# Kernel optimization log

Measured on AMD Instinct MI355X. Metric: run time of the kernel, lower is better.

The kernel has to match this reference:

```python
import jax, jax.numpy as jnp
import numpy as np

WINDOW = 11  # sliding window width (odd)


def setup_inputs() -> dict:
    key = jax.random.key(0)
    k1, k2, k3 = jax.random.split(key, 3)
    LENGTH, RANK = 200000, 64
    time_factor = jax.random.normal(k1, (LENGTH, RANK), dtype=jnp.float32)
    # nn.Linear(RANK, RANK): weight (out,in), bias (out,)
    W = jax.random.normal(k2, (RANK, RANK), dtype=jnp.float32) / np.sqrt(RANK)
    b = jax.random.normal(k3, (RANK,), dtype=jnp.float32) * 0.01
    return {"time_factor": time_factor, "W": W, "b": b}


def reference(time_factor, W, b):
    row, col = time_factor.shape
    pad = (WINDOW - 1) // 2
    # F.pad on transposed data pads the row (time) dimension with zeros
    padded = jnp.pad(time_factor, ((pad, pad), (0, 0)))
    # indexer: blocks[i] = padded[i : i+WINDOW]  -> (row, WINDOW, col)
    idx = jnp.arange(row)[:, None] + jnp.arange(WINDOW)[None, :]
    blocks = padded[idx]
    # var1 = tanh(Linear(data))  (exp contains '_tanh')
    var1 = jnp.tanh(time_factor @ W.T + b)            # (row, col)
    # var2 = bmm(blocks, var1) -> per-row window scores
    var2 = jnp.einsum('rwc,rc->rw', blocks, var1)      # (row, WINDOW)
    # exp ends with 'scaled'
    var2 = var2 / jnp.sqrt(jnp.asarray(col, time_factor.dtype))
    # exp starts with 'softmax' (softmax over window dim)
    var2 = jax.nn.softmax(var2, axis=1)
    # var3 = bmm(scores, blocks) -> smoothed factor
    out = jnp.einsum('rw,rwc->rc', var2, blocks)       # (row, col)
    return out
```

## Files before the change

kernel.cpp:

```cpp
#include <hip/hip_runtime.h>
#include <hip/hip_bf16.h>


constexpr int RANK   = 64;
constexpr int WINDOW = 11;
constexpr int PAD    = 5;
constexpr int TILE   = 16;
constexpr int BLOCK  = 256;
constexpr int TR     = 64;
constexpr int BROWS  = 28;
constexpr int BSTR   = 68;
constexpr int SC_S   = 18;
constexpr int GRIDB  = 1024;

constexpr int BAND_F = BROWS * BSTR;
constexpr int SC_OFF = 4 * BAND_F;
constexpr int SMEMF  = SC_OFF + 4 * 32 * SC_S;

typedef short short8  __attribute__((ext_vector_type(8)));
typedef float float4v __attribute__((ext_vector_type(4)));

__device__ __forceinline__ short8 cvt_bf8(float4 a, float4 b) {
    union { short8 s; __hip_bfloat162 h[4]; } u;
    u.h[0] = __float22bfloat162_rn(make_float2(a.x, a.y));
    u.h[1] = __float22bfloat162_rn(make_float2(a.z, a.w));
    u.h[2] = __float22bfloat162_rn(make_float2(b.x, b.y));
    u.h[3] = __float22bfloat162_rn(make_float2(b.z, b.w));
    return u.s;
}

__device__ __forceinline__ float fast_tanh(float x) {
    return 1.0f - 2.0f / (1.0f + __expf(2.0f * x));
}

__global__ __launch_bounds__(BLOCK)
__attribute__((amdgpu_waves_per_eu(4, 4)))
void attn_win_kernel(
    const float* __restrict__ A,
    const float* __restrict__ W,
    const float* __restrict__ b,
    float* __restrict__ out,
    int rows)
{
    __shared__ __align__(16) float smem[SMEMF];

    const int lane = threadIdx.x & 63;
    const int wv   = threadIdx.x >> 6;
    const int m16  = lane & 15;
    const int quad = lane >> 4;
    const int sr   = lane >> 4;
    const int sc4  = (lane & 15) * 4;

    float* const bandW = smem + wv * BAND_F;
    float* const ScW   = smem + SC_OFF + wv * 32 * SC_S;

    short8 wfrag[4][2];
    #pragma unroll
    for (int ct = 0; ct < 4; ct++) {
        #pragma unroll
        for (int kf = 0; kf < 2; kf++) {
            const float4* p =
                (const float4*)(W + (ct * 16 + m16) * RANK + kf * 32 + quad * 8);
            wfrag[ct][kf] = cvt_bf8(p[0], p[1]);
        }
    }
    float4 biasT[4];
    #pragma unroll
    for (int ct = 0; ct < 4; ct++)
        biasT[ct] = *(const float4*)(b + ct * 16 + quad * 4);

    const int idxA = 4 * m16 + 128 * (quad & 1);
    const int idxB = idxA + 64;

    const int n_btiles = (rows + TR - 1) / TR;
    int bt = blockIdx.x;
    if (bt >= n_btiles) return;

    {
        const int rw0 = bt * TR + wv * TILE;
        #pragma unroll
        for (int ro = 0; ro < 7; ro++) {
            const int g = rw0 - PAD + ro * 4 + sr;
            float4 x = make_float4(0.f, 0.f, 0.f, 0.f);
            if ((unsigned)g < (unsigned)rows)
                x = *(const float4*)(A + (size_t)g * RANK + sc4);
            *(float4*)&bandW[(ro * 4 + sr) * BSTR + sc4] = x;
        }
    }

    for (; bt < n_btiles; bt += gridDim.x) {
        const int rw = bt * TR + wv * TILE;

        short8 am1[2];
        #pragma unroll
        for (int kf = 0; kf < 2; kf++) {
            const float4* pp =
                (const float4*)&bandW[(PAD + m16) * BSTR + kf * 32 + quad * 8];
            am1[kf] = cvt_bf8(pp[0], pp[1]);
        }

        float4v accT[4];
        #pragma unroll
        for (int ct = 0; ct < 4; ct++)
            accT[ct] = (float4v){biasT[ct].x, biasT[ct].y,
                                 biasT[ct].z, biasT[ct].w};
        #pragma unroll
        for (int kf = 0; kf < 2; kf++)
            #pragma unroll
            for (int ct = 0; ct < 4; ct++)
                accT[ct] = __builtin_amdgcn_mfma_f32_16x16x32_bf16(
                    wfrag[ct][kf], am1[kf], accT[ct], 0, 0, 0);

        int pk[4][2];
        #pragma unroll
        for (int ct = 0; ct < 4; ct++)
            #pragma unroll
            for (int u = 0; u < 2; u++) {
                union { __hip_bfloat162 h; int i; } cv;
                cv.h = __float22bfloat162_rn(make_float2(
                    fast_tanh(accT[ct][2 * u]),
                    fast_tanh(accT[ct][2 * u + 1])));
                pk[ct][u] = cv.i;
            }

        short8 bfr[2];
        #pragma unroll
        for (int kf = 0; kf < 2; kf++) {
            union { int w[4]; short8 s; } u;
            #pragma unroll
            for (int w = 0; w < 4; w++) {
                const int idx = (w >> 1) ? idxB : idxA;
                const int lo = __builtin_amdgcn_ds_bpermute(idx, pk[2 * kf][w & 1]);
                const int hi = __builtin_amdgcn_ds_bpermute(idx, pk[2 * kf + 1][w & 1]);
                u.w[w] = (quad >= 2) ? hi : lo;
            }
            bfr[kf] = u.s;
        }

        short8 abnd[2][2];
        #pragma unroll
        for (int it = 0; it < 2; it++)
            #pragma unroll
            for (int kf = 0; kf < 2; kf++) {
                const float4* pp = (const float4*)
                    &bandW[(it * 16 + m16) * BSTR + kf * 32 + quad * 8];
                abnd[it][kf] = cvt_bf8(pp[0], pp[1]);
            }

        float4v sacc[2];
        sacc[0] = (float4v){0.f, 0.f, 0.f, 0.f};
        sacc[1] = (float4v){0.f, 0.f, 0.f, 0.f};
        #pragma unroll
        for (int kf = 0; kf < 2; kf++)
            #pragma unroll
            for (int it = 0; it < 2; it++)
                sacc[it] = __builtin_amdgcn_mfma_f32_16x16x32_bf16(
                    abnd[it][kf], bfr[kf], sacc[it], 0, 0, 0);

        #pragma unroll
        for (int it = 0; it < 2; it++)
            #pragma unroll
            for (int rg = 0; rg < 4; rg++)
                ScW[(it * 16 + quad * 4 + rg) * SC_S + m16] = sacc[it][rg];

        float4 stg[7];
        {
            const int rwn = rw + (int)gridDim.x * TR;
            #pragma unroll
            for (int ro = 0; ro < 7; ro++) {
                const int g = rwn - PAD + ro * 4 + sr;
                stg[ro] = make_float4(0.f, 0.f, 0.f, 0.f);
                if ((unsigned)g < (unsigned)rows)
                    stg[ro] = *(const float4*)(A + (size_t)g * RANK + sc4);
            }
        }

        float p[WINDOW];
        {
            float s[WINDOW];
            float mx = -1e30f;
            #pragma unroll
            for (int w = 0; w < WINDOW; w++) {
                s[w] = ScW[(m16 + w) * SC_S + m16];
                mx = fmaxf(mx, s[w]);
            }
            float den = 0.0f;
            #pragma unroll
            for (int w = 0; w < WINDOW; w++) {
                p[w] = __expf((s[w] - mx) * 0.125f);
                den += p[w];
            }
            const float rden = __fdividef(1.0f, den);
            #pragma unroll
            for (int w = 0; w < WINDOW; w++) p[w] *= rden;
        }

        float aw[26];
        #pragma unroll
        for (int s = 0; s < 26; s++) aw[s] = bandW[s * BSTR + lane];

        #pragma unroll
        for (int ro = 0; ro < 7; ro++)
            *(float4*)&bandW[(ro * 4 + sr) * BSTR + sc4] = stg[ro];

        #pragma unroll
        for (int rr = 0; rr < TILE; rr++) {
            float o = 0.0f;
            #pragma unroll
            for (int w = 0; w < WINDOW; w++) {
                const float pw = __uint_as_float(
                    __builtin_amdgcn_readlane(__float_as_uint(p[w]), rr));
                o = fmaf(pw, aw[rr + w], o);
            }
            if (rw + rr < rows)
                out[(size_t)(rw + rr) * RANK + lane] = o;
        }
    }
}

extern "C" void kernel_launch(void* const* d_in, const int* in_sizes, int n_in,
                              void* d_out, int out_size, void* d_ws, size_t ws_size,
                              hipStream_t stream) {
    const float* A = (const float*)d_in[0];
    const float* W = (const float*)d_in[1];
    const float* b = (const float*)d_in[2];
    float* out = (float*)d_out;

    const int rows     = in_sizes[0] / RANK;
    const int n_btiles = (rows + TR - 1) / TR;
    const int blocks   = n_btiles < GRIDB ? n_btiles : GRIDB;

    hipLaunchKernelGGL(attn_win_kernel, dim3(blocks), dim3(BLOCK), 0, stream,
                       A, W, b, out, rows);
}
```

Before: 120.4 us.

## Compute window softmax directly from MFMA accumulators, dropping the score LDS round-trip

The score MFMA results are no longer written to a shared-memory scratch tile and read back along the diagonal. Each lane masks out-of-window entries in its own accumulator registers, and the max and denominator are reduced across quads with xor shuffles. The final weighted sum then fetches each weight with readlane from the owning lane. This removes LDS traffic and the score scratch allocation, and the grid cap is raised at the same time. The cost is more exp work per lane, since each lane covers 8 candidate entries, plus extra shuffles and more complex lane indexing.

```diff
diff --git a/kernel.cpp b/kernel.cpp
--- a/kernel.cpp
+++ b/kernel.cpp
@@ -10,12 +10,10 @@
 constexpr int TR     = 64;
 constexpr int BROWS  = 28;
 constexpr int BSTR   = 68;
-constexpr int SC_S   = 18;
-constexpr int GRIDB  = 1024;
+constexpr int GRIDB  = 1280;
 
 constexpr int BAND_F = BROWS * BSTR;
-constexpr int SC_OFF = 4 * BAND_F;
-constexpr int SMEMF  = SC_OFF + 4 * 32 * SC_S;
+constexpr int SMEMF  = 4 * BAND_F + 4 * BSTR;
 
 typedef short short8  __attribute__((ext_vector_type(8)));
 typedef float float4v __attribute__((ext_vector_type(4)));
@@ -50,9 +48,9 @@
     const int quad = lane >> 4;
     const int sr   = lane >> 4;
     const int sc4  = (lane & 15) * 4;
+    const int dql  = quad * 4 - m16;
 
     float* const bandW = smem + wv * BAND_F;
-    float* const ScW   = smem + SC_OFF + wv * 32 * SC_S;
 
     short8 wfrag[4][2];
     #pragma unroll
@@ -147,22 +145,6 @@
                 abnd[it][kf] = cvt_bf8(pp[0], pp[1]);
             }
 
-        float4v sacc[2];
-        sacc[0] = (float4v){0.f, 0.f, 0.f, 0.f};
-        sacc[1] = (float4v){0.f, 0.f, 0.f, 0.f};
-        #pragma unroll
-        for (int kf = 0; kf < 2; kf++)
-            #pragma unroll
-            for (int it = 0; it < 2; it++)
-                sacc[it] = __builtin_amdgcn_mfma_f32_16x16x32_bf16(
-                    abnd[it][kf], bfr[kf], sacc[it], 0, 0, 0);
-
-        #pragma unroll
-        for (int it = 0; it < 2; it++)
-            #pragma unroll
-            for (int rg = 0; rg < 4; rg++)
-                ScW[(it * 16 + quad * 4 + rg) * SC_S + m16] = sacc[it][rg];
-
         float4 stg[7];
         {
             const int rwn = rw + (int)gridDim.x * TR;
@@ -175,25 +157,47 @@
             }
         }
 
-        float p[WINDOW];
-        {
-            float s[WINDOW];
-            float mx = -1e30f;
-            #pragma unroll
-            for (int w = 0; w < WINDOW; w++) {
-                s[w] = ScW[(m16 + w) * SC_S + m16];
-                mx = fmaxf(mx, s[w]);
-            }
-            float den = 0.0f;
-            #pragma unroll
-            for (int w = 0; w < WINDOW; w++) {
-                p[w] = __expf((s[w] - mx) * 0.125f);
-                den += p[w];
-            }
-            const float rden = __fdividef(1.0f, den);
-            #pragma unroll
-            for (int w = 0; w < WINDOW; w++) p[w] *= rden;
-        }
+        float4v sacc[2];
+        sacc[0] = (float4v){0.f, 0.f, 0.f, 0.f};
+        sacc[1] = (float4v){0.f, 0.f, 0.f, 0.f};
+        #pragma unroll
+        for (int kf = 0; kf < 2; kf++)
+            #pragma unroll
+            for (int it = 0; it < 2; it++)
+                sacc[it] = __builtin_amdgcn_mfma_f32_16x16x32_bf16(
+                    abnd[it][kf], bfr[kf], sacc[it], 0, 0, 0);
+
+        float sm[2][4];
+        float mx = -3.0e38f;
+        #pragma unroll
+        for (int it = 0; it < 2; it++)
+            #pragma unroll
+            for (int rg = 0; rg < 4; rg++) {
+                const int c = it * 16 + rg;
+                const bool in = (unsigned)(dql + c) <= 10u;
+                const float v = in ? sacc[it][rg] : -3.0e38f;
+                sm[it][rg] = v;
+                mx = fmaxf(mx, v);
+            }
+        mx = fmaxf(mx, __shfl_xor(mx, 16));
+        mx = fmaxf(mx, __shfl_xor(mx, 32));
+        float den = 0.0f;
+        #pragma unroll
+        for (int it = 0; it < 2; it++)
+            #pragma unroll
+            for (int rg = 0; rg < 4; rg++) {
+                const float e = __expf((sm[it][rg] - mx) * 0.125f);
+                sm[it][rg] = e;
+                den += e;
+            }
+        den += __shfl_xor(den, 16);
+        den += __shfl_xor(den, 32);
+        const float rden = __fdividef(1.0f, den);
+        #pragma unroll
+        for (int it = 0; it < 2; it++)
+            #pragma unroll
+            for (int rg = 0; rg < 4; rg++)
+                sm[it][rg] *= rden;
 
         float aw[26];
         #pragma unroll
@@ -208,8 +212,10 @@
             float o = 0.0f;
             #pragma unroll
             for (int w = 0; w < WINDOW; w++) {
-                const float pw = __uint_as_float(
-                    __builtin_amdgcn_readlane(__float_as_uint(p[w]), rr));
+                const int i  = rr + w;
+                const int ln = ((i & 15) >> 2) * 16 + rr;
+                const float pw = __uint_as_float(__builtin_amdgcn_readlane(
+                    __float_as_uint(sm[i >> 4][i & 3]), ln));
                 o = fmaf(pw, aw[rr + w], o);
             }
             if (rw + rr < rows)
```

Result: slower. 138.5 us (+15.0%).
